# Performance work log

Hardware: AMD Instinct MI355X
Metric: run time of the kernel (lower is better)

## Reference

```python
import jax, jax.numpy as jnp
import numpy as np

IN_FEATURES = 2048
OUT_FEATURES = 2048
BATCH = 4096


def setup_inputs() -> dict:
    key = jax.random.key(0)
    kx, kw, kb, kp = jax.random.split(key, 4)
    x = jax.random.normal(kx, (BATCH, IN_FEATURES), dtype=jnp.float32)
    weight = jax.random.normal(kw, (OUT_FEATURES, IN_FEATURES), dtype=jnp.float32)
    bias = jax.random.normal(kb, (OUT_FEATURES,), dtype=jnp.float32)
    # torch uses torch.randperm(in_features) at forward time; we fix a permutation here
    indices = jax.random.permutation(kp, IN_FEATURES).astype(jnp.int64)
    return {"x": x, "weight": weight, "bias": bias, "indices": indices}


def reference(x, weight, bias, indices):
    # Original: (x[:, None, :] * weight)[:, :, indices].sum(dim=2) + bias
    # Summing the permuted reduction axis == contracting the permuted operands;
    # we gather both x and weight along the permutation then do a real GEMM,
    # avoiding the huge [B, out, in] intermediate while keeping identical math.
    xp = x[:, indices]            # [B, in]
    wp = weight[:, indices]       # [out, in]
    return jnp.einsum('bi,oi->bo', xp, wp) + bias[None, :]
```

## Files before the change

kernel.cpp:

```cpp
#include <hip/hip_runtime.h>
#include <hip/hip_bf16.h>

#define M_DIM 4096
#define N_DIM 2048
#define K_DIM 2048

#define BM 128
#define BN 128
#define BK 64
#define NT (K_DIM / BK)
#define A_TILE (BM * BK)
#define B_TILE (BN * BK)

typedef __bf16 bf16x8 __attribute__((ext_vector_type(8)));
typedef float f32x4 __attribute__((ext_vector_type(4)));
typedef unsigned short u16x8 __attribute__((ext_vector_type(8)));

__device__ __forceinline__ unsigned short f32_to_bf16_rne(float f) {
  unsigned int u = __float_as_uint(f);
  u += 0x7fffu + ((u >> 16) & 1u);
  return (unsigned short)(u >> 16);
}

__global__ __launch_bounds__(256) void cvt_both(
    const float* __restrict__ x, const float* __restrict__ w,
    unsigned short* __restrict__ out, int xn8, int totn8) {
  int i = blockIdx.x * 256 + threadIdx.x;
  if (i >= totn8) return;
  const float* src = (i < xn8) ? (x + (size_t)i * 8)
                               : (w + (size_t)(i - xn8) * 8);
  f32x4 a = reinterpret_cast<const f32x4*>(src)[0];
  f32x4 b = reinterpret_cast<const f32x4*>(src)[1];
  u16x8 o;
  o[0] = f32_to_bf16_rne(a[0]); o[1] = f32_to_bf16_rne(a[1]);
  o[2] = f32_to_bf16_rne(a[2]); o[3] = f32_to_bf16_rne(a[3]);
  o[4] = f32_to_bf16_rne(b[0]); o[5] = f32_to_bf16_rne(b[1]);
  o[6] = f32_to_bf16_rne(b[2]); o[7] = f32_to_bf16_rne(b[3]);
  reinterpret_cast<u16x8*>(out)[i] = o;
}

__device__ __forceinline__ void gload_lds16(const unsigned short* g, unsigned short* l) {
  __builtin_amdgcn_global_load_lds(
      (const __attribute__((address_space(1))) unsigned int*)g,
      (__attribute__((address_space(3))) unsigned int*)l, 16, 0, 0);
}

#define LD8(p) (*reinterpret_cast<const bf16x8*>(p))
#define VMWAIT_(n) asm volatile("s_waitcnt vmcnt(" #n ")" ::: "memory")
#define VMWAIT(n) VMWAIT_(n)
#define SBAR() __builtin_amdgcn_s_barrier()
#define SCHED() __builtin_amdgcn_sched_barrier(0)

__global__ __launch_bounds__(256, 2) void gemm_db(
    const unsigned short* __restrict__ A,
    const unsigned short* __restrict__ B,
    const float* __restrict__ bias,
    float* __restrict__ C) {
  __shared__ unsigned short As[2 * A_TILE];
  __shared__ unsigned short Bs[2 * B_TILE];

  const int tid  = threadIdx.x;
  const int lane = tid & 63;
  const int wave = tid >> 6;
  const int wr   = wave >> 1;
  const int wc   = wave & 1;
  const int bn   = blockIdx.x;
  const int bm   = blockIdx.y;

  const int srow   = tid >> 3;
  const int schunk = (tid & 7) ^ (srow & 7);
  const unsigned short* Ag[4];
  const unsigned short* Bg[4];
#pragma unroll
  for (int j = 0; j < 4; ++j) {
    Ag[j] = A + (size_t)(bm * BM + j * 32 + srow) * K_DIM + schunk * 8;
    Bg[j] = B + (size_t)(bn * BN + j * 32 + srow) * K_DIM + schunk * 8;
  }

#define STAGE_ALL(buf, k0) do { \
    unsigned short* _da = &As[(buf) * A_TILE + tid * 8]; \
    unsigned short* _db = &Bs[(buf) * B_TILE + tid * 8]; \
    gload_lds16(Ag[0] + (k0), _da); \
    gload_lds16(Ag[1] + (k0), _da + 2048); \
    gload_lds16(Ag[2] + (k0), _da + 4096); \
    gload_lds16(Ag[3] + (k0), _da + 6144); \
    gload_lds16(Bg[0] + (k0), _db); \
    gload_lds16(Bg[1] + (k0), _db + 2048); \
    gload_lds16(Bg[2] + (k0), _db + 4096); \
    gload_lds16(Bg[3] + (k0), _db + 6144); \
  } while (0)

  const int fr = lane & 15;
  const int qq = lane >> 4;
  const int xr = fr & 7;
  int aoff[4][2], boff[4][2];
#pragma unroll
  for (int mi = 0; mi < 4; ++mi)
#pragma unroll
    for (int kk = 0; kk < 2; ++kk)
      aoff[mi][kk] = ((wr * 64 + mi * 16 + fr) * 8 + ((kk * 4 + qq) ^ xr)) * 8;
#pragma unroll
  for (int ni = 0; ni < 4; ++ni)
#pragma unroll
    for (int kk = 0; kk < 2; ++kk)
      boff[ni][kk] = ((wc * 64 + ni * 16 + fr) * 8 + ((kk * 4 + qq) ^ xr)) * 8;

  const f32x4 z = {0.f, 0.f, 0.f, 0.f};
  f32x4 acc[4][4];
#pragma unroll
  for (int i = 0; i < 4; ++i)
#pragma unroll
    for (int j = 0; j < 4; ++j) acc[i][j] = z;

  bf16x8 avA[4], bvA[4], avB[4], bvB[4];

#define READ_SET(av, bv, bufi, kk) do { \
    const unsigned short* Asb = &As[(bufi) * A_TILE]; \
    const unsigned short* Bsb = &Bs[(bufi) * B_TILE]; \
    bv[0] = LD8(Bsb + boff[0][kk]); bv[1] = LD8(Bsb + boff[1][kk]); \
    bv[2] = LD8(Bsb + boff[2][kk]); bv[3] = LD8(Bsb + boff[3][kk]); \
    av[0] = LD8(Asb + aoff[0][kk]); av[1] = LD8(Asb + aoff[1][kk]); \
    av[2] = LD8(Asb + aoff[2][kk]); av[3] = LD8(Asb + aoff[3][kk]); \
  } while (0)

#define MFMA_ALL(av, bv) do { \
    __builtin_amdgcn_s_setprio(1); \
    _Pragma("unroll") \
    for (int mi = 0; mi < 4; ++mi) { \
      acc[mi][0] = __builtin_amdgcn_mfma_f32_16x16x32_bf16(av[mi], bv[0], acc[mi][0], 0, 0, 0); \
      acc[mi][1] = __builtin_amdgcn_mfma_f32_16x16x32_bf16(av[mi], bv[1], acc[mi][1], 0, 0, 0); \
      acc[mi][2] = __builtin_amdgcn_mfma_f32_16x16x32_bf16(av[mi], bv[2], acc[mi][2], 0, 0, 0); \
      acc[mi][3] = __builtin_amdgcn_mfma_f32_16x16x32_bf16(av[mi], bv[3], acc[mi][3], 0, 0, 0); \
    } \
    __builtin_amdgcn_s_setprio(0); \
  } while (0)

#define TILE(p_, t_) do { \
    STAGE_ALL((p_) ^ 1, ((t_) + 1) * BK); \
    READ_SET(avB, bvB, p_, 1); \
    SCHED(); \
    MFMA_ALL(avA, bvA); \
    MFMA_ALL(avB, bvB); \
    SCHED(); \
    VMWAIT(0); \
    SBAR(); \
    SCHED(); \
    READ_SET(avA, bvA, (p_) ^ 1, 0); \
  } while (0)

  STAGE_ALL(0, 0);
  VMWAIT(0);
  SBAR();
  SCHED();
  READ_SET(avA, bvA, 0, 0);

#pragma unroll 1
  for (int s = 0; s < 15; ++s) {
    TILE(0, 2 * s);
    TILE(1, 2 * s + 1);
  }
  TILE(0, 30);

  READ_SET(avB, bvB, 1, 1);
  SCHED();
  MFMA_ALL(avA, bvA);
  MFMA_ALL(avB, bvB);

  const int orow0 = bm * BM + wr * 64 + qq * 4;
  const int ocol0 = bn * BN + wc * 64 + fr;
#pragma unroll
  for (int ni = 0; ni < 4; ++ni) {
    const int col = ocol0 + ni * 16;
    const float bv = bias[col];
#pragma unroll
    for (int mi = 0; mi < 4; ++mi) {
      const int row = orow0 + mi * 16;
#pragma unroll
      for (int r = 0; r < 4; ++r)
        C[(size_t)(row + r) * N_DIM + col] = acc[mi][ni][r] + bv;
    }
  }
#undef TILE
#undef MFMA_ALL
#undef READ_SET
#undef STAGE_ALL
}

__global__ __launch_bounds__(256) void gemm_f32_naive(
    const float* __restrict__ X, const float* __restrict__ W,
    const float* __restrict__ bias, float* __restrict__ C) {
  int o = blockIdx.x * 256 + threadIdx.x;
  if (o >= M_DIM * N_DIM) return;
  int m = o / N_DIM, n = o % N_DIM;
  const float* xr = X + (size_t)m * K_DIM;
  const float* wr = W + (size_t)n * K_DIM;
  float s = 0.f;
  for (int k = 0; k < K_DIM; ++k) s += xr[k] * wr[k];
  C[o] = s + bias[n];
}

extern "C" void kernel_launch(void* const* d_in, const int* in_sizes, int n_in,
                              void* d_out, int out_size, void* d_ws, size_t ws_size,
                              hipStream_t stream) {
  const float* x    = (const float*)d_in[0];
  const float* w    = (const float*)d_in[1];
  const float* bias = (const float*)d_in[2];
  float* out = (float*)d_out;

  const size_t x_elems = (size_t)M_DIM * K_DIM;
  const size_t w_elems = (size_t)N_DIM * K_DIM;
  const size_t need = (x_elems + w_elems) * sizeof(unsigned short);

  if (ws_size < need) {
    gemm_f32_naive<<<(M_DIM * N_DIM + 255) / 256, 256, 0, stream>>>(x, w, bias, out);
    return;
  }

  unsigned short* xb = (unsigned short*)d_ws;
  unsigned short* wb = xb + x_elems;

  const int xn8 = (int)(x_elems / 8);
  const int totn8 = (int)((x_elems + w_elems) / 8);
  cvt_both<<<(totn8 + 255) / 256, 256, 0, stream>>>(x, w, xb, xn8, totn8);

  dim3 grid(N_DIM / BN, M_DIM / BM);
  gemm_db<<<grid, 256, 0, stream>>>(xb, wb, bias, out);
}
```

Before: 53.34 us.

## Restructure GEMM to 2-wave blocks with BK=32 and XCD-aware tile remap

Result: slower. 59.86 us (+12.2%).

```diff
diff --git a/kernel.cpp b/kernel.cpp
--- a/kernel.cpp
+++ b/kernel.cpp
@@ -7,7 +7,7 @@
 
 #define BM 128
 #define BN 128
-#define BK 64
+#define BK 32
 #define NT (K_DIM / BK)
 #define A_TILE (BM * BK)
 #define B_TILE (BN * BK)
@@ -46,12 +46,11 @@
 }
 
 #define LD8(p) (*reinterpret_cast<const bf16x8*>(p))
-#define VMWAIT_(n) asm volatile("s_waitcnt vmcnt(" #n ")" ::: "memory")
-#define VMWAIT(n) VMWAIT_(n)
+#define VMWAIT0() asm volatile("s_waitcnt vmcnt(0)" ::: "memory")
 #define SBAR() __builtin_amdgcn_s_barrier()
 #define SCHED() __builtin_amdgcn_sched_barrier(0)
 
-__global__ __launch_bounds__(256, 2) void gemm_db(
+__global__ __launch_bounds__(128, 2) void gemm_4b(
     const unsigned short* __restrict__ A,
     const unsigned short* __restrict__ B,
     const float* __restrict__ bias,
@@ -61,14 +60,16 @@
 
   const int tid  = threadIdx.x;
   const int lane = tid & 63;
-  const int wave = tid >> 6;
-  const int wr   = wave >> 1;
-  const int wc   = wave & 1;
-  const int bn   = blockIdx.x;
-  const int bm   = blockIdx.y;
-
-  const int srow   = tid >> 3;
-  const int schunk = (tid & 7) ^ (srow & 7);
+  const int wc   = tid >> 6;
+
+  const int orig = blockIdx.x;
+  const int xcd  = orig & 7;
+  const int idx  = orig >> 3;
+  const int bm   = (xcd & 3) * 8 + (idx & 7);
+  const int bn   = (xcd >> 2) * 8 + (idx >> 3);
+
+  const int srow   = tid >> 2;
+  const int schunk = (tid & 3) ^ (srow & 3);
   const unsigned short* Ag[4];
   const unsigned short* Bg[4];
 #pragma unroll
@@ -77,56 +78,54 @@
     Bg[j] = B + (size_t)(bn * BN + j * 32 + srow) * K_DIM + schunk * 8;
   }
 
-#define STAGE_ALL(buf, k0) do { \
+#define STAGE(buf, k0) do { \
     unsigned short* _da = &As[(buf) * A_TILE + tid * 8]; \
     unsigned short* _db = &Bs[(buf) * B_TILE + tid * 8]; \
     gload_lds16(Ag[0] + (k0), _da); \
-    gload_lds16(Ag[1] + (k0), _da + 2048); \
-    gload_lds16(Ag[2] + (k0), _da + 4096); \
-    gload_lds16(Ag[3] + (k0), _da + 6144); \
+    gload_lds16(Ag[1] + (k0), _da + 1024); \
+    gload_lds16(Ag[2] + (k0), _da + 2048); \
+    gload_lds16(Ag[3] + (k0), _da + 3072); \
     gload_lds16(Bg[0] + (k0), _db); \
-    gload_lds16(Bg[1] + (k0), _db + 2048); \
-    gload_lds16(Bg[2] + (k0), _db + 4096); \
-    gload_lds16(Bg[3] + (k0), _db + 6144); \
+    gload_lds16(Bg[1] + (k0), _db + 1024); \
+    gload_lds16(Bg[2] + (k0), _db + 2048); \
+    gload_lds16(Bg[3] + (k0), _db + 3072); \
   } while (0)
 
   const int fr = lane & 15;
   const int qq = lane >> 4;
-  const int xr = fr & 7;
-  int aoff[4][2], boff[4][2];
-#pragma unroll
-  for (int mi = 0; mi < 4; ++mi)
-#pragma unroll
-    for (int kk = 0; kk < 2; ++kk)
-      aoff[mi][kk] = ((wr * 64 + mi * 16 + fr) * 8 + ((kk * 4 + qq) ^ xr)) * 8;
+  const int xr = fr & 3;
+  int aoff[8], boff[4];
+#pragma unroll
+  for (int mi = 0; mi < 8; ++mi)
+    aoff[mi] = ((mi * 16 + fr) * 4 + (qq ^ xr)) * 8;
 #pragma unroll
   for (int ni = 0; ni < 4; ++ni)
-#pragma unroll
-    for (int kk = 0; kk < 2; ++kk)
-      boff[ni][kk] = ((wc * 64 + ni * 16 + fr) * 8 + ((kk * 4 + qq) ^ xr)) * 8;
+    boff[ni] = ((wc * 64 + ni * 16 + fr) * 4 + (qq ^ xr)) * 8;
 
   const f32x4 z = {0.f, 0.f, 0.f, 0.f};
-  f32x4 acc[4][4];
-#pragma unroll
-  for (int i = 0; i < 4; ++i)
+  f32x4 acc[8][4];
+#pragma unroll
+  for (int i = 0; i < 8; ++i)
 #pragma unroll
     for (int j = 0; j < 4; ++j) acc[i][j] = z;
 
-  bf16x8 avA[4], bvA[4], avB[4], bvB[4];
-
-#define READ_SET(av, bv, bufi, kk) do { \
+  bf16x8 av[8], bv[4];
+
+#define READ_SET(bufi) do { \
     const unsigned short* Asb = &As[(bufi) * A_TILE]; \
     const unsigned short* Bsb = &Bs[(bufi) * B_TILE]; \
-    bv[0] = LD8(Bsb + boff[0][kk]); bv[1] = LD8(Bsb + boff[1][kk]); \
-    bv[2] = LD8(Bsb + boff[2][kk]); bv[3] = LD8(Bsb + boff[3][kk]); \
-    av[0] = LD8(Asb + aoff[0][kk]); av[1] = LD8(Asb + aoff[1][kk]); \
-    av[2] = LD8(Asb + aoff[2][kk]); av[3] = LD8(Asb + aoff[3][kk]); \
-  } while (0)
-
-#define MFMA_ALL(av, bv) do { \
+    bv[0] = LD8(Bsb + boff[0]); bv[1] = LD8(Bsb + boff[1]); \
+    bv[2] = LD8(Bsb + boff[2]); bv[3] = LD8(Bsb + boff[3]); \
+    av[0] = LD8(Asb + aoff[0]); av[1] = LD8(Asb + aoff[1]); \
+    av[2] = LD8(Asb + aoff[2]); av[3] = LD8(Asb + aoff[3]); \
+    av[4] = LD8(Asb + aoff[4]); av[5] = LD8(Asb + aoff[5]); \
+    av[6] = LD8(Asb + aoff[6]); av[7] = LD8(Asb + aoff[7]); \
+  } while (0)
+
+#define MFMA_ALL() do { \
     __builtin_amdgcn_s_setprio(1); \
     _Pragma("unroll") \
-    for (int mi = 0; mi < 4; ++mi) { \
+    for (int mi = 0; mi < 8; ++mi) { \
       acc[mi][0] = __builtin_amdgcn_mfma_f32_16x16x32_bf16(av[mi], bv[0], acc[mi][0], 0, 0, 0); \
       acc[mi][1] = __builtin_amdgcn_mfma_f32_16x16x32_bf16(av[mi], bv[1], acc[mi][1], 0, 0, 0); \
       acc[mi][2] = __builtin_amdgcn_mfma_f32_16x16x32_bf16(av[mi], bv[2], acc[mi][2], 0, 0, 0); \
@@ -135,55 +134,47 @@
     __builtin_amdgcn_s_setprio(0); \
   } while (0)
 
-#define TILE(p_, t_) do { \
-    STAGE_ALL((p_) ^ 1, ((t_) + 1) * BK); \
-    READ_SET(avB, bvB, p_, 1); \
-    SCHED(); \
-    MFMA_ALL(avA, bvA); \
-    MFMA_ALL(avB, bvB); \
-    SCHED(); \
-    VMWAIT(0); \
+#define ITER(p_, t_) do { \
+    STAGE((p_) ^ 1, ((t_) + 1) * BK); \
+    MFMA_ALL(); \
+    VMWAIT0(); \
     SBAR(); \
     SCHED(); \
-    READ_SET(avA, bvA, (p_) ^ 1, 0); \
-  } while (0)
-
-  STAGE_ALL(0, 0);
-  VMWAIT(0);
+    READ_SET((p_) ^ 1); \
+  } while (0)
+
+  STAGE(0, 0);
+  VMWAIT0();
   SBAR();
   SCHED();
-  READ_SET(avA, bvA, 0, 0);
+  READ_SET(0);
 
 #pragma unroll 1
-  for (int s = 0; s < 15; ++s) {
-    TILE(0, 2 * s);
-    TILE(1, 2 * s + 1);
-  }
-  TILE(0, 30);
-
-  READ_SET(avB, bvB, 1, 1);
-  SCHED();
-  MFMA_ALL(avA, bvA);
-  MFMA_ALL(avB, bvB);
-
-  const int orow0 = bm * BM + wr * 64 + qq * 4;
+  for (int s = 0; s < 31; ++s) {
+    ITER(0, 2 * s);
+    ITER(1, 2 * s + 1);
+  }
+  ITER(0, 62);
+  MFMA_ALL();
+
+  const int orow0 = bm * BM + qq * 4;
   const int ocol0 = bn * BN + wc * 64 + fr;
 #pragma unroll
   for (int ni = 0; ni < 4; ++ni) {
     const int col = ocol0 + ni * 16;
-    const float bv = bias[col];
-#pragma unroll
-    for (int mi = 0; mi < 4; ++mi) {
+    const float bvv = bias[col];
+#pragma unroll
+    for (int mi = 0; mi < 8; ++mi) {
       const int row = orow0 + mi * 16;
 #pragma unroll
       for (int r = 0; r < 4; ++r)
-        C[(size_t)(row + r) * N_DIM + col] = acc[mi][ni][r] + bv;
+        C[(size_t)(row + r) * N_DIM + col] = acc[mi][ni][r] + bvv;
     }
   }
-#undef TILE
+#undef ITER
 #undef MFMA_ALL
 #undef READ_SET
-#undef STAGE_ALL
+#undef STAGE
 }
 
 __global__ __launch_bounds__(256) void gemm_f32_naive(
@@ -223,6 +214,5 @@
   const int totn8 = (int)((x_elems + w_elems) / 8);
   cvt_both<<<(totn8 + 255) / 256, 256, 0, stream>>>(x, w, xb, xn8, totn8);
 
-  dim3 grid(N_DIM / BN, M_DIM / BM);
-  gemm_db<<<grid, 256, 0, stream>>>(xb, wb, bias, out);
-}
+  gemm_4b<<<512, 128, 0, stream>>>(xb, wb, bias, out);
+}
```
